# Performance work log

Measured on AMD Instinct MI355X. Metric: run time of the kernel, lower is better.

The kernel has to match this reference:

```python
import jax, jax.numpy as jnp
import numpy as np

VN, BN, NSW, EC, MN = 64, 200, 10, 63, 73
FIN, HID = 32, 64
VLOW, VUPP = 0.9, 1.1


def _ln(z, eps=1e-5):
    m = jnp.mean(z, axis=-1, keepdims=True)
    v = jnp.var(z, axis=-1, keepdims=True)
    return (z - m) * jax.lax.rsqrt(v + eps)


def _layer(x, s, conn, deg_inv, Ws, Wi, Wj, U, Vw, first):
    # dense gated edge update over (B,V,V,H)
    e = jnp.einsum('bvwh,hk->bvwk', s, Ws) + (x @ Wi)[:, :, None, :] + (x @ Wj)[:, None, :, :]
    e = jax.nn.relu(_ln(e))
    s_out = e if first else s + e
    gate = jax.nn.sigmoid(s_out) * conn[None, :, :, None]
    msg = jnp.einsum('bvwh,bwh->bvh', gate, x @ Vw) * deg_inv[None, :, None]  # mean agg
    h = jax.nn.relu(_ln(x @ U + msg))
    return (h if first else x + h), s_out


def setup_inputs() -> dict:
    key = jax.random.key(0)
    ks = jax.random.split(key, 24)
    # radial feeder: path graph (line edges) + long-range tie switches, i<j (triu)
    ea = np.stack([np.arange(VN - 1), np.arange(1, VN)]).astype(np.int32)
    es = np.stack([np.arange(NSW), np.arange(NSW) + 32]).astype(np.int32)
    A = np.zeros((VN, VN), np.float32); A[ea[0], ea[1]] = 1; A[ea[1], ea[0]] = 1
    S = np.zeros((VN, VN), np.float32); S[es[0], es[1]] = 1; S[es[1], es[0]] = 1
    par = np.concatenate([ea[0], es[0]]); chi = np.concatenate([ea[1], es[1]])
    Incp = np.zeros((VN, MN), np.float32); Incp[par, np.arange(MN)] = 1
    Incc = np.zeros((VN, MN), np.float32); Incc[chi, np.arange(MN)] = 1
    deg = (A + S).sum(1)
    Dinv = np.diag((1.0 / np.maximum(deg, 1.0)).astype(np.float32))

    def w(k, shape):
        return jax.random.normal(k, shape, jnp.float32) / np.sqrt(shape[-2])

    return {
        'x': jax.random.normal(ks[0], (BN, VN, FIN), jnp.float32),
        'A': jnp.asarray(A), 'S': jnp.asarray(S),
        'embed_s': jax.random.normal(ks[1], (2, FIN), jnp.float32),
        'p0_Ws': w(ks[2], (FIN, HID)), 'p0_Wi': w(ks[3], (FIN, HID)),
        'p0_Wj': w(ks[4], (FIN, HID)), 'p0_U': w(ks[5], (FIN, HID)),
        'p0_V': w(ks[6], (FIN, HID)),
        'pl_Ws': w(ks[7], (2, HID, HID)), 'pl_Wi': w(ks[8], (2, HID, HID)),
        'pl_Wj': w(ks[9], (2, HID, HID)), 'pl_U': w(ks[10], (2, HID, HID)),
        'pl_V': w(ks[11], (2, HID, HID)),
        'smlp_W1': w(ks[12], (4 * HID, 4 * HID)), 'smlp_W2': w(ks[13], (4 * HID, 4)),
        'cmlp_W1': w(ks[14], (3 * HID, 3 * HID)), 'cmlp_W2': w(ks[15], (3 * HID, 3)),
        'Dinv': jnp.asarray(Dinv), 'Incp': jnp.asarray(Incp), 'Incc': jnp.asarray(Incc),
        'edge_A': jnp.asarray(ea), 'edge_S': jnp.asarray(es),
    }


def reference(x, A, S, embed_s, p0_Ws, p0_Wi, p0_Wj, p0_U, p0_V,
              pl_Ws, pl_Wi, pl_Wj, pl_U, pl_V,
              smlp_W1, smlp_W2, cmlp_W1, cmlp_W2,
              Dinv, Incp, Incc, edge_A, edge_S):
    B = x.shape[0]
    conn = jnp.clip(A + S, 0.0, 1.0)                       # (V,V) union adjacency
    deg_inv = 1.0 / jnp.maximum(conn.sum(1), 1.0)
    # init_embed_edges over dense S -> (B,V,V,FIN)
    s = jnp.broadcast_to(embed_s[S.astype(jnp.int32)][None], (B, VN, VN, FIN))
    xh, s = _layer(x, s, conn, deg_inv, p0_Ws, p0_Wi, p0_Wj, p0_U, p0_V, True)
    for l in range(pl_Ws.shape[0]):
        xh, s = _layer(xh, s, conn, deg_inv, pl_Ws[l], pl_Wi[l], pl_Wj[l], pl_U[l], pl_V[l], False)
    x_g = xh.sum(1)                                        # (B,H) graph feature

    # -- switch head (gather at triu switch edges, identical across batch) --
    si, sj = edge_S[0], edge_S[1]
    xg_s = jnp.broadcast_to(x_g[:, None, :], (B, si.shape[0], HID))
    smlp_in = jnp.concatenate([s[:, si, sj, :], xh[:, si], xh[:, sj], xg_s], axis=-1)
    smlp_out = jax.nn.sigmoid(jax.nn.relu(smlp_in @ smlp_W1) @ smlp_W2)  # (B,nsw,4)
    topology = smlp_out[..., 0]
    graph_topo = jnp.concatenate([jnp.ones((B, MN - NSW), x.dtype), topology], axis=1)
    ps = smlp_out[..., 1] - 0.5
    vs_p = VLOW * (1 - smlp_out[..., 2]) + VUPP * smlp_out[..., 2]
    vs_c = VLOW * (1 - smlp_out[..., 3]) + VUPP * smlp_out[..., 3]

    # -- connection head (gather at triu line edges) --
    ai, aj = edge_A[0], edge_A[1]
    xg_c = jnp.broadcast_to(x_g[:, None, :], (B, ai.shape[0], HID))
    cmlp_in = jnp.concatenate([xh[:, ai], xh[:, aj], xg_c], axis=-1)
    cmlp_out = jax.nn.sigmoid(jax.nn.relu(cmlp_in @ cmlp_W1) @ cmlp_W2)  # (B,Ec,3)
    pc = cmlp_out[..., 0] - 0.5
    vc_p = VLOW * (1 - cmlp_out[..., 1]) + VUPP * cmlp_out[..., 1]
    vc_c = VLOW * (1 - cmlp_out[..., 2]) + VUPP * cmlp_out[..., 2]

    # scatter into (B,M) physics tensors: first M-nsw cols from CMLP, last nsw from SMLP
    p_flow = jnp.concatenate([pc, ps], axis=1)
    v_par = jnp.concatenate([vc_p, vs_p], axis=1)
    v_chi = jnp.concatenate([vc_c, vs_c], axis=1)
    v = v_par @ (Dinv @ Incp).T + v_chi @ (Dinv @ Incc).T   # (B,V)
    v = v.at[:, 0].set(1.0)
    return jnp.concatenate([p_flow, v, graph_topo], axis=1)  # (B, M+V+M)
```

## Files before the change

### kernel.cpp

```cpp
#include <hip/hip_runtime.h>

#define BN 200
#define VN 64
#define HIDD 64
#define FINN 32
#define NSW 10
#define EC 63
#define MNE 73
#define NEDGE 146
#define NPACK 128

typedef unsigned short u16;
typedef unsigned int u32;
typedef __attribute__((ext_vector_type(8))) short bf16x8;
typedef __attribute__((ext_vector_type(4))) float f32x4;

__device__ __forceinline__ float bfu(u16 u) { return __uint_as_float(((u32)u) << 16); }
__device__ __forceinline__ u16 f2bf(float f) {
    u32 x = __float_as_uint(f);
    u32 r = x + 0x7fffu + ((x >> 16) & 1u);
    return (u16)(r >> 16);
}
__device__ __forceinline__ float cvtv(const void* p, int i, int fl) {
    return fl ? bfu(((const u16*)p)[i]) : ((const float*)p)[i];
}

__device__ __forceinline__ float ln_relu64(float e) {
    float s1 = e, s2 = e * e;
#pragma unroll
    for (int m = 1; m < 64; m <<= 1) {
        s1 += __shfl_xor(s1, m);
        s2 += __shfl_xor(s2, m);
    }
    float mean = s1 * 0.015625f;
    float var = fmaxf(s2 * 0.015625f - mean * mean, 0.f);
    return fmaxf((e - mean) * rsqrtf(var + 1e-5f), 0.f);
}

__device__ __forceinline__ void split8(const float* base, bf16x8* hi, bf16x8* lo) {
    union { bf16x8 v; u16 s[8]; } uh, ul;
#pragma unroll
    for (int j = 0; j < 8; j++) {
        float f = base[j];
        u16 h = f2bf(f);
        uh.s[j] = h;
        ul.s[j] = f2bf(f - bfu(h));
    }
    *hi = uh.v;
    *lo = ul.v;
}

struct CvtArgs { const void* src[21]; };

__global__ __launch_bounds__(256) void k_prep(CvtArgs ca, const int* __restrict__ eA,
                                              const int* __restrict__ eS,
                                              u16* __restrict__ c1h, u16* __restrict__ c1l,
                                              u16* __restrict__ c2h, u16* __restrict__ c2l,
                                              u16* __restrict__ s1h, u16* __restrict__ s1l,
                                              u16* __restrict__ s2h, u16* __restrict__ s2l,
                                              u16* __restrict__ w0h, u16* __restrict__ w0l,
                                              u16* __restrict__ wlh, u16* __restrict__ wll,
                                              float* __restrict__ ews, float* __restrict__ dinv,
                                              int* __restrict__ row_ptr, int* __restrict__ colp,
                                              int* __restrict__ sw_eidx,
                                              float* __restrict__ dinvD, int* __restrict__ incCnt,
                                              int* __restrict__ incM) {
    int t = threadIdx.x;
    int fl = (((const u16*)ca.src[1])[1] == 0x3F80) ? 1 : 0;
    if (blockIdx.x == 0) {
        __shared__ unsigned char flagL[64 * 65];
        __shared__ float wsL[FINN * 64];
        __shared__ float emL[64];
        __shared__ int degL[64], rpS[65], colS[NEDGE + 16];
        __shared__ int eAL[2 * EC], eSL[2 * NSW];

        if (t < 2 * EC) eAL[t] = eA[t];
        if (t >= 128 && t < 128 + 2 * NSW) eSL[t - 128] = eS[t - 128];
        if (t >= 160 && t < 224) emL[t - 160] = cvtv(ca.src[3], t - 160, fl);
        for (int i = t; i < FINN * 64; i += 256) wsL[i] = cvtv(ca.src[4], i, fl);
        for (int i = t; i < 4096; i += 256) {
            float a = cvtv(ca.src[1], i, fl);
            float s = cvtv(ca.src[2], i, fl);
            int r = i >> 6, c = i & 63;
            flagL[r * 65 + c] = (unsigned char)(((a != 0.f || s != 0.f) ? 1 : 0) |
                                                ((s != 0.f) ? 2 : 0));
        }
        __syncthreads();

        if (t < 128) {
            int j = t >> 6, k = t & 63;
            float a = 0.f;
#pragma unroll
            for (int h = 0; h < FINN; h++) a += emL[j * FINN + h] * wsL[h * 64 + k];
            ews[(j << 6) + k] = a;
        }
        if (t < 64) {
            int d = 0;
#pragma unroll
            for (int w = 0; w < 64; w++) d += flagL[t * 65 + w] & 1;
            degL[t] = d;
            dinv[t] = 1.f / fmaxf((float)d, 1.f);
        }
        __syncthreads();
        if (t == 0) {
            int c = 0;
            for (int v = 0; v < 64; v++) { rpS[v] = c; c += degL[v]; }
            rpS[64] = c;
        }
        __syncthreads();
        if (t < 65) row_ptr[t] = rpS[t];
        if (t < 64) {
            int pos = rpS[t];
#pragma unroll
            for (int w = 0; w < 64; w++) {
                int f = flagL[t * 65 + w];
                if (f & 1) colS[pos++] = w | ((f & 2) ? 256 : 0);
            }
        }
        __syncthreads();
        int tot = rpS[64];
        if (t < tot) colp[t] = colS[t];
        if (t < NSW) {
            int si = eSL[t], sj = eSL[NSW + t];
            int idx = 0;
            for (int e = rpS[si]; e < rpS[si + 1]; e++)
                if ((colS[e] & 255) == sj) idx = e;
            sw_eidx[t] = idx;
        }
        if (t < 64) {
            dinvD[t] = cvtv(ca.src[18], t * 64 + t, fl);
            int cnt = 0;
            for (int m = 0; m < MNE; m++) {
                int par = (m < EC) ? eAL[m] : eSL[m - EC];
                int chi = (m < EC) ? eAL[EC + m] : eSL[NSW + (m - EC)];
                if (par == t && cnt < 8) incM[t * 8 + cnt++] = (m << 1);
                if (chi == t && cnt < 8) incM[t * 8 + cnt++] = (m << 1) | 1;
            }
            incCnt[t] = cnt;
        }
    } else {
        const int T1 = 36864, T2 = T1 + 3072, T3 = T2 + 65536, T4 = T3 + 4096;
        const int T5 = T4 + 8192, TOT = T5 + 40960;
        for (int i = (blockIdx.x - 1) * 256 + t; i < TOT; i += NPACK * 256) {
            int idx = i;
            const void* src;
            u16 *dh, *dl;
            int K2, N2, nt, rem, loff = 0;
            if (idx < T1) {
                nt = idx / 3072; rem = idx - nt * 3072; src = ca.src[16];
                dh = c1h + idx; dl = c1l + idx; K2 = 192; N2 = 192;
            } else if (idx < T2) {
                idx -= T1; nt = 0; rem = idx; src = ca.src[17];
                dh = c2h + idx; dl = c2l + idx; K2 = 192; N2 = 3;
            } else if (idx < T3) {
                idx -= T2; nt = idx >> 12; rem = idx & 4095; src = ca.src[14];
                dh = s1h + idx; dl = s1l + idx; K2 = 256; N2 = 256;
            } else if (idx < T4) {
                idx -= T3; nt = 0; rem = idx; src = ca.src[15];
                dh = s2h + idx; dl = s2l + idx; K2 = 256; N2 = 4;
            } else if (idx < T5) {
                int j = idx - T4;
                int mt = j >> 11;
                int m2 = j & 2047;
                nt = m2 >> 9; rem = m2 & 511; src = ca.src[5 + mt];
                dh = w0h + j; dl = w0l + j; K2 = 32; N2 = 64;
            } else {
                int j = idx - T5;
                int l = j / 20480;
                int jj = j - l * 20480;
                int mt = jj >> 12;
                int m2 = jj & 4095;
                nt = m2 >> 10; rem = m2 & 1023; src = ca.src[9 + mt];
                loff = l * 4096;
                dh = wlh + j; dl = wll + j; K2 = 64; N2 = 64;
            }
            int kb = rem >> 9, r8 = rem & 511, ln = r8 >> 3, jq = r8 & 7;
            int k = kb * 32 + ((ln >> 4) << 3) + jq;
            int n = nt * 16 + (ln & 15);
            float val = 0.f;
            if (n < N2 && k < K2) val = cvtv(src, loff + k * N2 + n, fl);
            u16 h = f2bf(val);
            *dh = h;
            *dl = f2bf(val - bfu(h));
        }
    }
}

#define XI 0
#define XJ 1
#define XU 2
#define XV 3
#define CSTR 204
#define SSTR 268

__global__ __launch_bounds__(1024) void k_main(
    const void* __restrict__ xraw, const u16* __restrict__ A_u16,
    const int* __restrict__ eA, const int* __restrict__ eS,
    const float* __restrict__ ews, const float* __restrict__ dinv,
    const int* __restrict__ row_ptr, const int* __restrict__ colp,
    const int* __restrict__ sw_eidx,
    const float* __restrict__ dinvD, const int* __restrict__ incCnt, const int* __restrict__ incM,
    const u16* __restrict__ w0h, const u16* __restrict__ w0l,
    const u16* __restrict__ wlh, const u16* __restrict__ wll,
    const u16* __restrict__ c1h, const u16* __restrict__ c1l,
    const u16* __restrict__ c2h, const u16* __restrict__ c2l,
    const u16* __restrict__ s1h, const u16* __restrict__ s1l,
    const u16* __restrict__ s2h, const u16* __restrict__ s2l,
    void* __restrict__ out_v)
{
    __shared__ float xL[64 * 64];
    __shared__ float sL[NEDGE * 64];
    __shared__ float preL[NEDGE * 64];
    __shared__ float tLs[4 * 64 * 64];
    __shared__ float xgL[64];
    __shared__ float ewsL[128];
    __shared__ float dinvL[64];
    __shared__ int rpL[65];
    __shared__ int colL[NEDGE + 6];
    __shared__ int swL[NSW];
    __shared__ float cmoL[EC * 3];
    __shared__ float smoL[NSW * 4];

    int b = blockIdx.x, t = threadIdx.x;
    int lane = t & 63, wid = t >> 6;
    int m = lane & 15, quad = lane >> 4;
    int fl = (A_u16[1] == 0x3F80) ? 1 : 0;

    for (int i = t; i < 2048; i += 1024) {
        int r = i >> 5, c = i & 31;
        xL[(r << 6) + c] = cvtv(xraw, b * 2048 + i, fl);
    }
    if (t < 128) ewsL[t] = ews[t];
    if (t < 64) dinvL[t] = dinv[t];
    if (t < 65) rpL[t] = row_ptr[t];
    if (t < NEDGE) colL[t] = colp[t];
    if (t < NSW) swL[t] = sw_eidx[t];
    __syncthreads();

    {
        int mat = wid >> 2, Mt = wid & 3;
        const u16* bhp = w0h + mat * 2048;
        const u16* blp = w0l + mat * 2048;
        int row = Mt * 16 + m;
        bf16x8 ah, al;
        split8(&xL[(row << 6) + quad * 8], &ah, &al);
        f32x4 acc[4];
#pragma unroll
        for (int nt = 0; nt < 4; nt++) acc[nt] = (f32x4){0.f, 0.f, 0.f, 0.f};
#pragma unroll
        for (int nt = 0; nt < 4; nt++) {
            int o = (nt << 9) + (lane << 3);
            bf16x8 bh = *(const bf16x8*)(bhp + o);
            bf16x8 bl = *(const bf16x8*)(blp + o);
            acc[nt] = __builtin_amdgcn_mfma_f32_16x16x32_bf16(ah, bh, acc[nt], 0, 0, 0);
            acc[nt] = __builtin_amdgcn_mfma_f32_16x16x32_bf16(al, bh, acc[nt], 0, 0, 0);
            acc[nt] = __builtin_amdgcn_mfma_f32_16x16x32_bf16(ah, bl, acc[nt], 0, 0, 0);
        }
#pragma unroll
        for (int nt = 0; nt < 4; nt++)
#pragma unroll
            for (int r = 0; r < 4; r++)
                tLs[mat * 4096 + ((Mt * 16 + quad * 4 + r) << 6) + nt * 16 + m] = acc[nt][r];
    }
    __syncthreads();

    {
#pragma unroll
        for (int q = 0; q < 4; q++) {
            int v = (wid << 2) + q;
            int e0 = rpL[v], e1 = rpL[v + 1];
            float xival = tLs[XI * 4096 + (v << 6) + lane];
            float macc = 0.f;
            for (int e = e0; e < e1; e++) {
                int cp = colL[e];
                int w = cp & 255;
                float ee = ewsL[(((cp >> 8) & 1) << 6) + lane] + xival
                         + tLs[XJ * 4096 + (w << 6) + lane];
                float sout = ln_relu64(ee);
                sL[(e << 6) + lane] = sout;
                macc += tLs[XV * 4096 + (w << 6) + lane] / (1.f + __expf(-sout));
            }
            float z = tLs[XU * 4096 + (v << 6) + lane] + macc * dinvL[v];
            xL[(v << 6) + lane] = ln_relu64(z);
        }
    }
    __syncthreads();

    for (int l = 0; l < 2; l++) {
        {
            int mat = wid >> 2, Mt = wid & 3;
            const u16* bhp = wlh + l * 20480 + (mat + 1) * 4096;
            const u16* blp = wll + l * 20480 + (mat + 1) * 4096;
            int row = Mt * 16 + m;
            f32x4 acc[4];
#pragma unroll
            for (int nt = 0; nt < 4; nt++) acc[nt] = (f32x4){0.f, 0.f, 0.f, 0.f};
#pragma unroll
            for (int kb = 0; kb < 2; kb++) {
                bf16x8 ah, al;
                split8(&xL[(row << 6) + kb * 32 + quad * 8], &ah, &al);
#pragma unroll
                for (int nt = 0; nt < 4; nt++) {
                    int o = (((nt << 1) + kb) << 9) + (lane << 3);
                    bf16x8 bh = *(const bf16x8*)(bhp + o);
                    bf16x8 bl = *(const bf16x8*)(blp + o);
                    acc[nt] = __builtin_amdgcn_mfma_f32_16x16x32_bf16(ah, bh, acc[nt], 0, 0, 0);
                    acc[nt] = __builtin_amdgcn_mfma_f32_16x16x32_bf16(al, bh, acc[nt], 0, 0, 0);
                    acc[nt] = __builtin_amdgcn_mfma_f32_16x16x32_bf16(ah, bl, acc[nt], 0, 0, 0);
                }
            }
#pragma unroll
            for (int nt = 0; nt < 4; nt++)
#pragma unroll
                for (int r = 0; r < 4; r++)
                    tLs[mat * 4096 + ((Mt * 16 + quad * 4 + r) << 6) + nt * 16 + m] = acc[nt][r];

            if (wid < 10) {
                const u16* sbh = wlh + l * 20480;
                const u16* sbl = wll + l * 20480;
                int srow = wid * 16 + m;
                int ar = (srow > NEDGE - 1) ? (NEDGE - 1) : srow;
                f32x4 sacc[4];
#pragma unroll
                for (int nt = 0; nt < 4; nt++) sacc[nt] = (f32x4){0.f, 0.f, 0.f, 0.f};
#pragma unroll
                for (int kb = 0; kb < 2; kb++) {
                    bf16x8 ah, al;
                    split8(&sL[(ar << 6) + kb * 32 + quad * 8], &ah, &al);
#pragma unroll
                    for (int nt = 0; nt < 4; nt++) {
                        int o = (((nt << 1) + kb) << 9) + (lane << 3);
                        bf16x8 bh = *(const bf16x8*)(sbh + o);
                        bf16x8 bl = *(const bf16x8*)(sbl + o);
                        sacc[nt] = __builtin_amdgcn_mfma_f32_16x16x32_bf16(ah, bh, sacc[nt], 0, 0, 0);
                        sacc[nt] = __builtin_amdgcn_mfma_f32_16x16x32_bf16(al, bh, sacc[nt], 0, 0, 0);
                        sacc[nt] = __builtin_amdgcn_mfma_f32_16x16x32_bf16(ah, bl, sacc[nt], 0, 0, 0);
                    }
                }
#pragma unroll
                for (int nt = 0; nt < 4; nt++)
#pragma unroll
                    for (int r = 0; r < 4; r++) {
                        int orow = wid * 16 + quad * 4 + r;
                        if (orow < NEDGE)
                            preL[(orow << 6) + nt * 16 + m] = sacc[nt][r];
                    }
            }
        }
        __syncthreads();

        {
#pragma unroll
            for (int q = 0; q < 4; q++) {
                int v = (wid << 2) + q;
                int e0 = rpL[v], e1 = rpL[v + 1];
                float xival = tLs[XI * 4096 + (v << 6) + lane];
                float macc = 0.f;
                for (int e = e0; e < e1; e++) {
                    int cp = colL[e];
                    int w = cp & 255;
                    float ee = preL[(e << 6) + lane] + xival
                             + tLs[XJ * 4096 + (w << 6) + lane];
                    float sout = sL[(e << 6) + lane] + ln_relu64(ee);
                    sL[(e << 6) + lane] = sout;
                    macc += tLs[XV * 4096 + (w << 6) + lane] / (1.f + __expf(-sout));
                }
                float z = tLs[XU * 4096 + (v << 6) + lane] + macc * dinvL[v];
                float h = ln_relu64(z);
                xL[(v << 6) + lane] += h;
            }
        }
        __syncthreads();
    }

    float* hidF = tLs;
    float* xgP = preL;

    {
        float a = 0.f;
#pragma unroll
        for (int q = 0; q < 4; q++)
            a += xL[(((wid << 2) + q) << 6) + lane];
        xgP[wid * 64 + lane] = a;
    }
    __syncthreads();
    if (t < 64) {
        float s = 0.f;
#pragma unroll
        for (int i = 0; i < 16; i++) s += xgP[i * 64 + t];
        xgL[t] = s;
    }
    __syncthreads();

    {
        int Mt = wid >> 2, ntb = wid & 3;
        int e = Mt * 16 + m; if (e > 62) e = 62;
        int ai = eA[e], aj = eA[EC + e];
        const float* seg0 = xL + (ai << 6);
        const float* seg1 = xL + (aj << 6);
        const float* seg2 = xgL;
        f32x4 acc[3];
#pragma unroll
        for (int j3 = 0; j3 < 3; j3++) acc[j3] = (f32x4){0.f, 0.f, 0.f, 0.f};
#pragma unroll
        for (int kb = 0; kb < 6; kb++) {
            int k = kb * 32 + quad * 8;
            const float* base = (k < 64) ? seg0 + k : (k < 128) ? seg1 + (k - 64) : seg2 + (k - 128);
            bf16x8 ah, al;
            split8(base, &ah, &al);
#pragma unroll
            for (int j3 = 0; j3 < 3; j3++) {
                int nt = ntb + j3 * 4;
                int o = ((nt * 6 + kb) << 9) + (lane << 3);
                bf16x8 bh = *(const bf16x8*)(c1h + o);
                bf16x8 bl = *(const bf16x8*)(c1l + o);
                acc[j3] = __builtin_amdgcn_mfma_f32_16x16x32_bf16(ah, bh, acc[j3], 0, 0, 0);
                acc[j3] = __builtin_amdgcn_mfma_f32_16x16x32_bf16(al, bh, acc[j3], 0, 0, 0);
                acc[j3] = __builtin_amdgcn_mfma_f32_16x16x32_bf16(ah, bl, acc[j3], 0, 0, 0);
            }
        }
#pragma unroll
        for (int j3 = 0; j3 < 3; j3++) {
            int nt = ntb + j3 * 4;
#pragma unroll
            for (int r = 0; r < 4; r++)
                hidF[(Mt * 16 + quad * 4 + r) * CSTR + nt * 16 + m] = fmaxf(acc[j3][r], 0.f);
        }
    }
    __syncthreads();

    if (wid < 4) {
        f32x4 accD = (f32x4){0.f, 0.f, 0.f, 0.f};
#pragma unroll
        for (int kb = 0; kb < 6; kb++) {
            bf16x8 ah, al;
            split8(&hidF[(wid * 16 + m) * CSTR + kb * 32 + quad * 8], &ah, &al);
            int o = (kb << 9) + (lane << 3);
            bf16x8 bh = *(const bf16x8*)(c2h + o);
            bf16x8 bl = *(const bf16x8*)(c2l + o);
            accD = __builtin_amdgcn_mfma_f32_16x16x32_bf16(ah, bh, accD, 0, 0, 0);
            accD = __builtin_amdgcn_mfma_f32_16x16x32_bf16(al, bh, accD, 0, 0, 0);
            accD = __builtin_amdgcn_mfma_f32_16x16x32_bf16(ah, bl, accD, 0, 0, 0);
        }
#pragma unroll
        for (int r = 0; r < 4; r++) {
            int row = wid * 16 + quad * 4 + r;
            if (row < EC && m < 3)
                cmoL[row * 3 + m] = 1.f / (1.f + __expf(-accD[r]));
        }
    }
    __syncthreads();

    {
        int e2 = (m > 9) ? 9 : m;
        int si = eS[e2], sj = eS[NSW + e2];
        int sw = swL[e2];
        const float* t0 = sL + (sw << 6);
        const float* t1 = xL + (si << 6);
        const float* t2 = xL + (sj << 6);
        const float* t3 = xgL;
        f32x4 accS = (f32x4){0.f, 0.f, 0.f, 0.f};
#pragma unroll
        for (int kb = 0; kb < 8; kb++) {
            int k = kb * 32 + quad * 8;
            const float* base = (k < 64) ? t0 + k : (k < 128) ? t1 + (k - 64)
                              : (k < 192) ? t2 + (k - 128) : t3 + (k - 192);
            bf16x8 ah, al;
            split8(base, &ah, &al);
            int o = ((wid * 8 + kb) << 9) + (lane << 3);
            bf16x8 bh = *(const bf16x8*)(s1h + o);
            bf16x8 bl = *(const bf16x8*)(s1l + o);
            accS = __builtin_amdgcn_mfma_f32_16x16x32_bf16(ah, bh, accS, 0, 0, 0);
            accS = __builtin_amdgcn_mfma_f32_16x16x32_bf16(al, bh, accS, 0, 0, 0);
            accS = __builtin_amdgcn_mfma_f32_16x16x32_bf16(ah, bl, accS, 0, 0, 0);
        }
#pragma unroll
        for (int r = 0; r < 4; r++)
            hidF[(quad * 4 + r) * SSTR + wid * 16 + m] = fmaxf(accS[r], 0.f);
    }
    __syncthreads();

    if (wid == 0) {
        f32x4 accT = (f32x4){0.f, 0.f, 0.f, 0.f};
#pragma unroll
        for (int kb = 0; kb < 8; kb++) {
            bf16x8 ah, al;
            split8(&hidF[m * SSTR + kb * 32 + quad * 8], &ah, &al);
            int o = (kb << 9) + (lane << 3);
            bf16x8 bh = *(const bf16x8*)(s2h + o);
            bf16x8 bl = *(const bf16x8*)(s2l + o);
            accT = __builtin_amdgcn_mfma_f32_16x16x32_bf16(ah, bh, accT, 0, 0, 0);
            accT = __builtin_amdgcn_mfma_f32_16x16x32_bf16(al, bh, accT, 0, 0, 0);
            accT = __builtin_amdgcn_mfma_f32_16x16x32_bf16(ah, bl, accT, 0, 0, 0);
        }
#pragma unroll
        for (int r = 0; r < 4; r++) {
            int row = quad * 4 + r;
            if (row < NSW && m < 4)
                smoL[row * 4 + m] = 1.f / (1.f + __expf(-accT[r]));
        }
    }
    __syncthreads();

    if (t < 2 * MNE + VN) {
        float val;
        if (t < MNE) {
            val = (t < EC) ? cmoL[t * 3] - 0.5f : smoL[(t - EC) * 4 + 1] - 0.5f;
        } else if (t < MNE + VN) {
            int i = t - MNE;
            if (i == 0) {
                val = 1.0f;
            } else {
                float acc = 0.f;
                int c = incCnt[i];
                for (int q = 0; q < c; q++) {
                    int em = incM[i * 8 + q];
                    int mm = em >> 1, role = em & 1;
                    float vv = (mm < EC) ? 0.9f + 0.2f * cmoL[mm * 3 + 1 + role]
                                         : 0.9f + 0.2f * smoL[(mm - EC) * 4 + 2 + role];
                    acc += vv;
                }
                val = acc * dinvD[i];
            }
        } else {
            int mm = t - (MNE + VN);
            val = (mm < EC) ? 1.0f : smoL[(mm - EC) * 4];
        }
        size_t oidx = (size_t)b * (2 * MNE + VN) + t;
        if (fl) ((u16*)out_v)[oidx] = f2bf(val);
        else    ((float*)out_v)[oidx] = val;
    }
}

extern "C" void kernel_launch(void* const* d_in, const int* in_sizes, int n_in,
                              void* d_out, int out_size, void* d_ws, size_t ws_size,
                              hipStream_t stream) {
    const int* eA = (const int*)d_in[21];
    const int* eS = (const int*)d_in[22];

    float* pool = (float*)d_ws;
    float* ews     = pool;
    float* dinv    = ews + 128;
    float* dinvD   = dinv + 64;
    int*   row_ptr = (int*)(dinvD + 64);
    int*   colp    = row_ptr + 80;
    int*   sw_eidx = colp + 256;
    int*   incCnt  = sw_eidx + 16;
    int*   incM    = incCnt + 64;
    u16*   c1h = (u16*)(incM + 512);
    u16*   c1l = c1h + 36864;
    u16*   c2h = c1l + 36864;
    u16*   c2l = c2h + 3072;
    u16*   s1h = c2l + 3072;
    u16*   s1l = s1h + 65536;
    u16*   s2h = s1l + 65536;
    u16*   s2l = s2h + 4096;
    u16*   w0h = s2l + 4096;
    u16*   w0l = w0h + 8192;
    u16*   wlh = w0l + 8192;
    u16*   wll = wlh + 40960;

    CvtArgs ca;
    for (int i = 0; i < 21; i++) ca.src[i] = d_in[i];

    k_prep<<<1 + NPACK, 256, 0, stream>>>(ca, eA, eS,
                                          c1h, c1l, c2h, c2l, s1h, s1l, s2h, s2l,
                                          w0h, w0l, wlh, wll,
                                          ews, dinv, row_ptr, colp, sw_eidx,
                                          dinvD, incCnt, incM);

    k_main<<<BN, 1024, 0, stream>>>(d_in[0], (const u16*)d_in[1], eA, eS,
                                    ews, dinv, row_ptr, colp, sw_eidx,
                                    dinvD, incCnt, incM,
                                    w0h, w0l, wlh, wll,
                                    c1h, c1l, c2h, c2l, s1h, s1l, s2h, s2l,
                                    d_out);
}
```

Before: 171.7 us.

## Store shared activations as pre-split swizzled bf16 hi/lo pairs

```diff
diff --git a/kernel.cpp b/kernel.cpp
--- a/kernel.cpp
+++ b/kernel.cpp
@@ -25,6 +25,17 @@
     return fl ? bfu(((const u16*)p)[i]) : ((const float*)p)[i];
 }
 
+__device__ __forceinline__ int swz(int row, int col) { return col ^ ((row & 7) << 3); }
+
+__device__ __forceinline__ float ldp(const u16* H, const u16* L, int idx) {
+    return bfu(H[idx]) + bfu(L[idx]);
+}
+__device__ __forceinline__ void stp(u16* H, u16* L, int idx, float f) {
+    u16 h = f2bf(f);
+    H[idx] = h;
+    L[idx] = f2bf(f - bfu(h));
+}
+
 __device__ __forceinline__ float ln_relu64(float e) {
     float s1 = e, s2 = e * e;
 #pragma unroll
@@ -35,19 +46,6 @@
     float mean = s1 * 0.015625f;
     float var = fmaxf(s2 * 0.015625f - mean * mean, 0.f);
     return fmaxf((e - mean) * rsqrtf(var + 1e-5f), 0.f);
-}
-
-__device__ __forceinline__ void split8(const float* base, bf16x8* hi, bf16x8* lo) {
-    union { bf16x8 v; u16 s[8]; } uh, ul;
-#pragma unroll
-    for (int j = 0; j < 8; j++) {
-        float f = base[j];
-        u16 h = f2bf(f);
-        uh.s[j] = h;
-        ul.s[j] = f2bf(f - bfu(h));
-    }
-    *hi = uh.v;
-    *lo = ul.v;
 }
 
 struct CvtArgs { const void* src[21]; };
@@ -190,8 +188,6 @@
 #define XJ 1
 #define XU 2
 #define XV 3
-#define CSTR 204
-#define SSTR 268
 
 __global__ __launch_bounds__(1024) void k_main(
     const void* __restrict__ xraw, const u16* __restrict__ A_u16,
@@ -208,18 +204,17 @@
     const u16* __restrict__ s2h, const u16* __restrict__ s2l,
     void* __restrict__ out_v)
 {
-    __shared__ float xL[64 * 64];
-    __shared__ float sL[NEDGE * 64];
-    __shared__ float preL[NEDGE * 64];
-    __shared__ float tLs[4 * 64 * 64];
-    __shared__ float xgL[64];
+    __shared__ __align__(16) u16 xHp[64 * 64], xLp[64 * 64];
+    __shared__ __align__(16) u16 sHp[NEDGE * 64], sLp[NEDGE * 64];
+    __shared__ __align__(16) float preL[NEDGE * 64];
+    __shared__ __align__(16) float tLs[4 * 64 * 64];
+    __shared__ __align__(16) u16 xgH[64], xgLo[64];
     __shared__ float ewsL[128];
     __shared__ float dinvL[64];
     __shared__ int rpL[65];
     __shared__ int colL[NEDGE + 6];
-    __shared__ int swL[NSW];
-    __shared__ float cmoL[EC * 3];
-    __shared__ float smoL[NSW * 4];
+    __shared__ int swLx[NSW];
+    __shared__ float cmoL[EC * 3], smoL[NSW * 4];
 
     int b = blockIdx.x, t = threadIdx.x;
     int lane = t & 63, wid = t >> 6;
@@ -228,13 +223,13 @@
 
     for (int i = t; i < 2048; i += 1024) {
         int r = i >> 5, c = i & 31;
-        xL[(r << 6) + c] = cvtv(xraw, b * 2048 + i, fl);
+        stp(xHp, xLp, (r << 6) + swz(r, c), cvtv(xraw, b * 2048 + i, fl));
     }
     if (t < 128) ewsL[t] = ews[t];
     if (t < 64) dinvL[t] = dinv[t];
     if (t < 65) rpL[t] = row_ptr[t];
     if (t < NEDGE) colL[t] = colp[t];
-    if (t < NSW) swL[t] = sw_eidx[t];
+    if (t < NSW) swLx[t] = sw_eidx[t];
     __syncthreads();
 
     {
@@ -242,8 +237,9 @@
         const u16* bhp = w0h + mat * 2048;
         const u16* blp = w0l + mat * 2048;
         int row = Mt * 16 + m;
-        bf16x8 ah, al;
-        split8(&xL[(row << 6) + quad * 8], &ah, &al);
+        int c0 = quad * 8;
+        bf16x8 ah = *(const bf16x8*)&xHp[(row << 6) + swz(row, c0)];
+        bf16x8 al = *(const bf16x8*)&xLp[(row << 6) + swz(row, c0)];
         f32x4 acc[4];
 #pragma unroll
         for (int nt = 0; nt < 4; nt++) acc[nt] = (f32x4){0.f, 0.f, 0.f, 0.f};
@@ -259,8 +255,10 @@
 #pragma unroll
         for (int nt = 0; nt < 4; nt++)
 #pragma unroll
-            for (int r = 0; r < 4; r++)
-                tLs[mat * 4096 + ((Mt * 16 + quad * 4 + r) << 6) + nt * 16 + m] = acc[nt][r];
+            for (int r = 0; r < 4; r++) {
+                int orow = Mt * 16 + quad * 4 + r;
+                tLs[mat * 4096 + (orow << 6) + swz(orow, nt * 16 + m)] = acc[nt][r];
+            }
     }
     __syncthreads();
 
@@ -269,19 +267,19 @@
         for (int q = 0; q < 4; q++) {
             int v = (wid << 2) + q;
             int e0 = rpL[v], e1 = rpL[v + 1];
-            float xival = tLs[XI * 4096 + (v << 6) + lane];
+            float xival = tLs[XI * 4096 + (v << 6) + swz(v, lane)];
             float macc = 0.f;
             for (int e = e0; e < e1; e++) {
                 int cp = colL[e];
                 int w = cp & 255;
                 float ee = ewsL[(((cp >> 8) & 1) << 6) + lane] + xival
-                         + tLs[XJ * 4096 + (w << 6) + lane];
+                         + tLs[XJ * 4096 + (w << 6) + swz(w, lane)];
                 float sout = ln_relu64(ee);
-                sL[(e << 6) + lane] = sout;
-                macc += tLs[XV * 4096 + (w << 6) + lane] / (1.f + __expf(-sout));
-            }
-            float z = tLs[XU * 4096 + (v << 6) + lane] + macc * dinvL[v];
-            xL[(v << 6) + lane] = ln_relu64(z);
+                stp(sHp, sLp, (e << 6) + swz(e, lane), sout);
+                macc += tLs[XV * 4096 + (w << 6) + swz(w, lane)] / (1.f + __expf(-sout));
+            }
+            float z = tLs[XU * 4096 + (v << 6) + swz(v, lane)] + macc * dinvL[v];
+            stp(xHp, xLp, (v << 6) + swz(v, lane), ln_relu64(z));
         }
     }
     __syncthreads();
@@ -297,8 +295,9 @@
             for (int nt = 0; nt < 4; nt++) acc[nt] = (f32x4){0.f, 0.f, 0.f, 0.f};
 #pragma unroll
             for (int kb = 0; kb < 2; kb++) {
-                bf16x8 ah, al;
-                split8(&xL[(row << 6) + kb * 32 + quad * 8], &ah, &al);
+                int c0 = kb * 32 + quad * 8;
+                bf16x8 ah = *(const bf16x8*)&xHp[(row << 6) + swz(row, c0)];
+                bf16x8 al = *(const bf16x8*)&xLp[(row << 6) + swz(row, c0)];
 #pragma unroll
                 for (int nt = 0; nt < 4; nt++) {
                     int o = (((nt << 1) + kb) << 9) + (lane << 3);
@@ -312,8 +311,10 @@
 #pragma unroll
             for (int nt = 0; nt < 4; nt++)
 #pragma unroll
-                for (int r = 0; r < 4; r++)
-                    tLs[mat * 4096 + ((Mt * 16 + quad * 4 + r) << 6) + nt * 16 + m] = acc[nt][r];
+                for (int r = 0; r < 4; r++) {
+                    int orow = Mt * 16 + quad * 4 + r;
+                    tLs[mat * 4096 + (orow << 6) + swz(orow, nt * 16 + m)] = acc[nt][r];
+                }
 
             if (wid < 10) {
                 const u16* sbh = wlh + l * 20480;
@@ -325,8 +326,9 @@
                 for (int nt = 0; nt < 4; nt++) sacc[nt] = (f32x4){0.f, 0.f, 0.f, 0.f};
 #pragma unroll
                 for (int kb = 0; kb < 2; kb++) {
-                    bf16x8 ah, al;
-                    split8(&sL[(ar << 6) + kb * 32 + quad * 8], &ah, &al);
+                    int c0 = kb * 32 + quad * 8;
+                    bf16x8 ah = *(const bf16x8*)&sHp[(ar << 6) + swz(ar, c0)];
+                    bf16x8 al = *(const bf16x8*)&sLp[(ar << 6) + swz(ar, c0)];
 #pragma unroll
                     for (int nt = 0; nt < 4; nt++) {
                         int o = (((nt << 1) + kb) << 9) + (lane << 3);
@@ -343,7 +345,7 @@
                     for (int r = 0; r < 4; r++) {
                         int orow = wid * 16 + quad * 4 + r;
                         if (orow < NEDGE)
-                            preL[(orow << 6) + nt * 16 + m] = sacc[nt][r];
+                            preL[(orow << 6) + swz(orow, nt * 16 + m)] = sacc[nt][r];
                     }
             }
         }
@@ -354,33 +356,41 @@
             for (int q = 0; q < 4; q++) {
                 int v = (wid << 2) + q;
                 int e0 = rpL[v], e1 = rpL[v + 1];
-                float xival = tLs[XI * 4096 + (v << 6) + lane];
+                float xival = tLs[XI * 4096 + (v << 6) + swz(v, lane)];
                 float macc = 0.f;
                 for (int e = e0; e < e1; e++) {
                     int cp = colL[e];
                     int w = cp & 255;
-                    float ee = preL[(e << 6) + lane] + xival
-                             + tLs[XJ * 4096 + (w << 6) + lane];
-                    float sout = sL[(e << 6) + lane] + ln_relu64(ee);
-                    sL[(e << 6) + lane] = sout;
-                    macc += tLs[XV * 4096 + (w << 6) + lane] / (1.f + __expf(-sout));
+                    int sidx = (e << 6) + swz(e, lane);
+                    float ee = preL[sidx] + xival
+                             + tLs[XJ * 4096 + (w << 6) + swz(w, lane)];
+                    float sout = ldp(sHp, sLp, sidx) + ln_relu64(ee);
+                    stp(sHp, sLp, sidx, sout);
+                    macc += tLs[XV * 4096 + (w << 6) + swz(w, lane)] / (1.f + __expf(-sout));
                 }
-                float z = tLs[XU * 4096 + (v << 6) + lane] + macc * dinvL[v];
+                float z = tLs[XU * 4096 + (v << 6) + swz(v, lane)] + macc * dinvL[v];
                 float h = ln_relu64(z);
-                xL[(v << 6) + lane] += h;
+                int xidx = (v << 6) + swz(v, lane);
+                stp(xHp, xLp, xidx, ldp(xHp, xLp, xidx) + h);
             }
         }
         __syncthreads();
     }
 
-    float* hidF = tLs;
+    u16* tp  = (u16*)tLs;
+    u16* hcH = tp;
+    u16* hcL = tp + 12288;
+    u16* hsH = tp + 24576;
+    u16* hsL = tp + 28672;
     float* xgP = preL;
 
     {
         float a = 0.f;
 #pragma unroll
-        for (int q = 0; q < 4; q++)
-            a += xL[(((wid << 2) + q) << 6) + lane];
+        for (int q = 0; q < 4; q++) {
+            int r = (wid << 2) + q;
+            a += ldp(xHp, xLp, (r << 6) + swz(r, lane));
+        }
         xgP[wid * 64 + lane] = a;
     }
     __syncthreads();
@@ -388,7 +398,7 @@
         float s = 0.f;
 #pragma unroll
         for (int i = 0; i < 16; i++) s += xgP[i * 64 + t];
-        xgL[t] = s;
+        stp(xgH, xgLo, t, s);
     }
     __syncthreads();
 
@@ -396,18 +406,25 @@
         int Mt = wid >> 2, ntb = wid & 3;
         int e = Mt * 16 + m; if (e > 62) e = 62;
         int ai = eA[e], aj = eA[EC + e];
-        const float* seg0 = xL + (ai << 6);
-        const float* seg1 = xL + (aj << 6);
-        const float* seg2 = xgL;
         f32x4 acc[3];
 #pragma unroll
         for (int j3 = 0; j3 < 3; j3++) acc[j3] = (f32x4){0.f, 0.f, 0.f, 0.f};
 #pragma unroll
         for (int kb = 0; kb < 6; kb++) {
             int k = kb * 32 + quad * 8;
-            const float* base = (k < 64) ? seg0 + k : (k < 128) ? seg1 + (k - 64) : seg2 + (k - 128);
             bf16x8 ah, al;
-            split8(base, &ah, &al);
+            if (k < 64) {
+                ah = *(const bf16x8*)&xHp[(ai << 6) + swz(ai, k)];
+                al = *(const bf16x8*)&xLp[(ai << 6) + swz(ai, k)];
+            } else if (k < 128) {
+                int c = k - 64;
+                ah = *(const bf16x8*)&xHp[(aj << 6) + swz(aj, c)];
+                al = *(const bf16x8*)&xLp[(aj << 6) + swz(aj, c)];
+            } else {
+                int c = k - 128;
+                ah = *(const bf16x8*)&xgH[c];
+                al = *(const bf16x8*)&xgLo[c];
+            }
 #pragma unroll
             for (int j3 = 0; j3 < 3; j3++) {
                 int nt = ntb + j3 * 4;
@@ -419,22 +436,27 @@
                 acc[j3] = __builtin_amdgcn_mfma_f32_16x16x32_bf16(ah, bl, acc[j3], 0, 0, 0);
             }
         }
+        __syncthreads();
 #pragma unroll
         for (int j3 = 0; j3 < 3; j3++) {
             int nt = ntb + j3 * 4;
 #pragma unroll
-            for (int r = 0; r < 4; r++)
-                hidF[(Mt * 16 + quad * 4 + r) * CSTR + nt * 16 + m] = fmaxf(acc[j3][r], 0.f);
+            for (int r = 0; r < 4; r++) {
+                int row = Mt * 16 + quad * 4 + r;
+                stp(hcH, hcL, row * 192 + swz(row, nt * 16 + m), fmaxf(acc[j3][r], 0.f));
+            }
         }
     }
     __syncthreads();
 
     if (wid < 4) {
         f32x4 accD = (f32x4){0.f, 0.f, 0.f, 0.f};
+        int row = wid * 16 + m;
 #pragma unroll
         for (int kb = 0; kb < 6; kb++) {
-            bf16x8 ah, al;
-            split8(&hidF[(wid * 16 + m) * CSTR + kb * 32 + quad * 8], &ah, &al);
+            int c0 = kb * 32 + quad * 8;
+            bf16x8 ah = *(const bf16x8*)&hcH[row * 192 + swz(row, c0)];
+            bf16x8 al = *(const bf16x8*)&hcL[row * 192 + swz(row, c0)];
             int o = (kb << 9) + (lane << 3);
             bf16x8 bh = *(const bf16x8*)(c2h + o);
             bf16x8 bl = *(const bf16x8*)(c2l + o);
@@ -444,9 +466,9 @@
         }
 #pragma unroll
         for (int r = 0; r < 4; r++) {
-            int row = wid * 16 + quad * 4 + r;
-            if (row < EC && m < 3)
-                cmoL[row * 3 + m] = 1.f / (1.f + __expf(-accD[r]));
+            int row2 = wid * 16 + quad * 4 + r;
+            if (row2 < EC && m < 3)
+                cmoL[row2 * 3 + m] = 1.f / (1.f + __expf(-accD[r]));
         }
     }
     __syncthreads();
@@ -454,19 +476,28 @@
     {
         int e2 = (m > 9) ? 9 : m;
         int si = eS[e2], sj = eS[NSW + e2];
-        int sw = swL[e2];
-        const float* t0 = sL + (sw << 6);
-        const float* t1 = xL + (si << 6);
-        const float* t2 = xL + (sj << 6);
-        const float* t3 = xgL;
+        int sw = swLx[e2];
         f32x4 accS = (f32x4){0.f, 0.f, 0.f, 0.f};
 #pragma unroll
         for (int kb = 0; kb < 8; kb++) {
             int k = kb * 32 + quad * 8;
-            const float* base = (k < 64) ? t0 + k : (k < 128) ? t1 + (k - 64)
-                              : (k < 192) ? t2 + (k - 128) : t3 + (k - 192);
             bf16x8 ah, al;
-            split8(base, &ah, &al);
+            if (k < 64) {
+                ah = *(const bf16x8*)&sHp[(sw << 6) + swz(sw, k)];
+                al = *(const bf16x8*)&sLp[(sw << 6) + swz(sw, k)];
+            } else if (k < 128) {
+                int c = k - 64;
+                ah = *(const bf16x8*)&xHp[(si << 6) + swz(si, c)];
+                al = *(const bf16x8*)&xLp[(si << 6) + swz(si, c)];
+            } else if (k < 192) {
+                int c = k - 128;
+                ah = *(const bf16x8*)&xHp[(sj << 6) + swz(sj, c)];
+                al = *(const bf16x8*)&xLp[(sj << 6) + swz(sj, c)];
+            } else {
+                int c = k - 192;
+                ah = *(const bf16x8*)&xgH[c];
+                al = *(const bf16x8*)&xgLo[c];
+            }
             int o = ((wid * 8 + kb) << 9) + (lane << 3);
             bf16x8 bh = *(const bf16x8*)(s1h + o);
             bf16x8 bl = *(const bf16x8*)(s1l + o);
@@ -475,8 +506,10 @@
             accS = __builtin_amdgcn_mfma_f32_16x16x32_bf16(ah, bl, accS, 0, 0, 0);
         }
 #pragma unroll
-        for (int r = 0; r < 4; r++)
-            hidF[(quad * 4 + r) * SSTR + wid * 16 + m] = fmaxf(accS[r], 0.f);
+        for (int r = 0; r < 4; r++) {
+            int row = quad * 4 + r;
+            stp(hsH, hsL, (row << 8) + swz(row, wid * 16 + m), fmaxf(accS[r], 0.f));
+        }
     }
     __syncthreads();
 
@@ -484,8 +517,9 @@
         f32x4 accT = (f32x4){0.f, 0.f, 0.f, 0.f};
 #pragma unroll
         for (int kb = 0; kb < 8; kb++) {
-            bf16x8 ah, al;
-            split8(&hidF[m * SSTR + kb * 32 + quad * 8], &ah, &al);
+            int c0 = kb * 32 + quad * 8;
+            bf16x8 ah = *(const bf16x8*)&hsH[(m << 8) + swz(m, c0)];
+            bf16x8 al = *(const bf16x8*)&hsL[(m << 8) + swz(m, c0)];
             int o = (kb << 9) + (lane << 3);
             bf16x8 bh = *(const bf16x8*)(s2h + o);
             bf16x8 bl = *(const bf16x8*)(s2l + o);
```

New measurement: 177.1 us. +3.1%, slower.
